# Kernel optimization log

Measured on AMD Instinct MI355X. Metric: run time of the kernel, lower is better.

## Reference

```python
import jax, jax.numpy as jnp
import numpy as np

D_DIM = 100000  # vocabulary size
W_DIM = 128     # embedding width
BATCH = 4096    # number of (center, context) index pairs


def setup_inputs() -> dict:
    key = jax.random.key(0)
    k1, k2, kw1, kb1, kw2, kb2 = jax.random.split(key, 6)
    idx1 = jax.random.randint(k1, (BATCH,), 0, D_DIM, dtype=jnp.int64 if jax.config.jax_enable_x64 else jnp.int32)
    idx2 = jax.random.randint(k2, (BATCH,), 0, D_DIM, dtype=jnp.int64 if jax.config.jax_enable_x64 else jnp.int32)
    # torch.nn.Linear(D, W): weight [W, D], bias [W], uniform(-1/sqrt(D), 1/sqrt(D))
    bound = 1.0 / np.sqrt(D_DIM)
    W1 = jax.random.uniform(kw1, (W_DIM, D_DIM), jnp.float32, -bound, bound)
    b1 = jax.random.uniform(kb1, (W_DIM,), jnp.float32, -bound, bound)
    W2 = jax.random.uniform(kw2, (W_DIM, D_DIM), jnp.float32, -bound, bound)
    b2 = jax.random.uniform(kb2, (W_DIM,), jnp.float32, -bound, bound)
    return {"idx1": idx1, "idx2": idx2, "W1": W1, "b1": b1, "W2": W2, "b2": b2}


def reference(idx1, idx2, W1, b1, W2, b2):
    # Linear(one_hot(idx)) == weight[:, idx] + bias  -> direct row (column) gather.
    p1 = W1[:, idx1].T + b1              # [B, W_dim]
    p2 = W2[:, idx2].T + b2              # [B, W_dim]
    s = jax.nn.sigmoid(jnp.sum(p1 * p2, axis=-1))  # [B]
    # original: cat([1 - sigmoid, sigmoid]) -> [B, 2]
    return jnp.stack([1.0 - s, s], axis=-1)
```

## Files before the change

### kernel.cpp

```cpp
#include <hip/hip_runtime.h>
#include <math.h>

#define D_DIM 100000
#define W_DIM 128
#define BATCH 4096

__global__ __launch_bounds__(256) void sgns_kernel(
    const int* __restrict__ idx1,
    const int* __restrict__ idx2,
    const float* __restrict__ W1,
    const float* __restrict__ b1,
    const float* __restrict__ W2,
    const float* __restrict__ b2,
    float* __restrict__ out)
{
    const int gtid = blockIdx.x * blockDim.x + threadIdx.x;
    const int wave = gtid >> 6;
    const int lane = gtid & 63;
    if (wave >= BATCH) return;

    const int i1 = idx1[wave];
    const int i2 = idx2[wave];

    const int w0 = lane;
    const int w1 = lane + 64;

    const float a0 = W1[w0 * D_DIM + i1];
    const float a1 = W1[w1 * D_DIM + i1];
    const float c0 = W2[w0 * D_DIM + i2];
    const float c1 = W2[w1 * D_DIM + i2];

    const float p0 = a0 + b1[w0];
    const float p1 = a1 + b1[w1];
    const float q0 = c0 + b2[w0];
    const float q1 = c1 + b2[w1];

    float v = p0 * q0 + p1 * q1;

    #pragma unroll
    for (int off = 32; off > 0; off >>= 1)
        v += __shfl_down(v, off, 64);

    if (lane == 0) {
        const float s = 1.0f / (1.0f + expf(-v));
        out[wave * 2 + 0] = 1.0f - s;
        out[wave * 2 + 1] = s;
    }
}

extern "C" void kernel_launch(void* const* d_in, const int* in_sizes, int n_in,
                              void* d_out, int out_size, void* d_ws, size_t ws_size,
                              hipStream_t stream)
{
    const int*   idx1 = (const int*)  d_in[0];
    const int*   idx2 = (const int*)  d_in[1];
    const float* W1   = (const float*)d_in[2];
    const float* b1   = (const float*)d_in[3];
    const float* W2   = (const float*)d_in[4];
    const float* b2   = (const float*)d_in[5];
    float* out = (float*)d_out;

    const int threads = 256;
    const int blocks  = (BATCH * 64) / threads;
    sgns_kernel<<<blocks, threads, 0, stream>>>(idx1, idx2, W1, b1, W2, b2, out);
}
```

Before: 125.3 us.

## Stream weight rows through LDS and gather indices, then reduce in second kernel

Replaces the scattered column gather with a two-kernel scheme. The first kernel streams contiguous chunks of each weight row into shared memory with coalesced float4 loads, then scatters the matching gathered values plus bias into a transposed workspace. The second kernel computes the dot products and the sigmoid from the workspace. This turns a random-access gather, where each element costs its own cache line, into a full sequential read of both weight matrices (about 102 MB). It adds a workspace round trip and a second launch, and the bandwidth cost no longer depends on batch size.

```diff
diff --git a/kernel.cpp b/kernel.cpp
--- a/kernel.cpp
+++ b/kernel.cpp
@@ -4,47 +4,70 @@
 #define D_DIM 100000
 #define W_DIM 128
 #define BATCH 4096
+#define CH    12288
+#define NCH   9
 
-__global__ __launch_bounds__(256) void sgns_kernel(
-    const int* __restrict__ idx1,
-    const int* __restrict__ idx2,
-    const float* __restrict__ W1,
-    const float* __restrict__ b1,
-    const float* __restrict__ W2,
-    const float* __restrict__ b2,
+__global__ __launch_bounds__(256) void gather_rows(
+    const int* __restrict__ idx1, const int* __restrict__ idx2,
+    const float* __restrict__ W1, const float* __restrict__ b1,
+    const float* __restrict__ W2, const float* __restrict__ b2,
+    float* __restrict__ G1T, float* __restrict__ G2T)
+{
+    __shared__ float lds[CH];
+
+    const int bid = blockIdx.x;
+    const int m   = bid / (W_DIM * NCH);
+    const int rem = bid % (W_DIM * NCH);
+    const int w   = rem / NCH;
+    const int c   = rem % NCH;
+
+    const float* __restrict__ W   = m ? W2   : W1;
+    const int*   __restrict__ idx = m ? idx2 : idx1;
+    const float  bias             = m ? b2[w] : b1[w];
+    float* __restrict__ GT        = m ? G2T  : G1T;
+
+    const int base  = c * CH;
+    const int limit = min(CH, D_DIM - base);
+    const float* src = W + (size_t)w * D_DIM + base;
+
+    const int n4 = limit >> 2;
+    const float4* __restrict__ src4 = (const float4*)src;
+    float4* lds4 = (float4*)lds;
+    for (int i = threadIdx.x; i < n4; i += 256)
+        lds4[i] = src4[i];
+    __syncthreads();
+
+    for (int b = threadIdx.x; b < BATCH; b += 256) {
+        const int rel = idx[b] - base;
+        if ((unsigned)rel < (unsigned)limit)
+            GT[w * BATCH + b] = lds[rel] + bias;
+    }
+}
+
+__global__ __launch_bounds__(256) void dot_sig(
+    const float* __restrict__ G1T, const float* __restrict__ G2T,
     float* __restrict__ out)
 {
-    const int gtid = blockIdx.x * blockDim.x + threadIdx.x;
-    const int wave = gtid >> 6;
-    const int lane = gtid & 63;
-    if (wave >= BATCH) return;
+    __shared__ float red[8][32];
+    const int bl = threadIdx.x & 31;
+    const int sl = threadIdx.x >> 5;
+    const int b  = blockIdx.x * 32 + bl;
 
-    const int i1 = idx1[wave];
-    const int i2 = idx2[wave];
+    float acc = 0.0f;
+    #pragma unroll
+    for (int k = 0; k < 16; ++k) {
+        const int w = sl * 16 + k;
+        acc += G1T[w * BATCH + b] * G2T[w * BATCH + b];
+    }
+    red[sl][bl] = acc;
+    __syncthreads();
 
-    const int w0 = lane;
-    const int w1 = lane + 64;
-
-    const float a0 = W1[w0 * D_DIM + i1];
-    const float a1 = W1[w1 * D_DIM + i1];
-    const float c0 = W2[w0 * D_DIM + i2];
-    const float c1 = W2[w1 * D_DIM + i2];
-
-    const float p0 = a0 + b1[w0];
-    const float p1 = a1 + b1[w1];
-    const float q0 = c0 + b2[w0];
-    const float q1 = c1 + b2[w1];
-
-    float v = p0 * q0 + p1 * q1;
-
-    #pragma unroll
-    for (int off = 32; off > 0; off >>= 1)
-        v += __shfl_down(v, off, 64);
-
-    if (lane == 0) {
-        const float s = 1.0f / (1.0f + expf(-v));
-        out[wave * 2 + 0] = 1.0f - s;
-        out[wave * 2 + 1] = s;
+    if (sl == 0) {
+        float v = 0.0f;
+        #pragma unroll
+        for (int s = 0; s < 8; ++s) v += red[s][bl];
+        const float sgm = 1.0f / (1.0f + expf(-v));
+        ((float2*)out)[b] = make_float2(1.0f - sgm, sgm);
     }
 }
 
@@ -60,7 +83,9 @@
     const float* b2   = (const float*)d_in[5];
     float* out = (float*)d_out;
 
-    const int threads = 256;
-    const int blocks  = (BATCH * 64) / threads;
-    sgns_kernel<<<blocks, threads, 0, stream>>>(idx1, idx2, W1, b1, W2, b2, out);
+    float* G1T = (float*)d_ws;
+    float* G2T = G1T + (size_t)W_DIM * BATCH;
+
+    gather_rows<<<2 * W_DIM * NCH, 256, 0, stream>>>(idx1, idx2, W1, b1, W2, b2, G1T, G2T);
+    dot_sig<<<BATCH / 32, 256, 0, stream>>>(G1T, G2T, out);
 }
```

Measured after the change: 151.9 us. +21.3%, slower.

## Bucket-sort indices to cluster column gathers, then split gather and dot into kernels

Applied to the files above, without the earlier changes.

Adds a single-block counting sort per index array that buckets indices by value (16 consecutive columns per bucket), so the gather kernel visits nearby columns of the weight matrices together and shares the 64-byte cache lines they touch. The gather kernel writes the biased embedding rows into a workspace buffer, and a separate kernel computes the dot product and sigmoid. The block order is swizzled to spread work. This costs two extra launches, a serial sort on only two blocks, and a round trip of 4 MB through the workspace buffer.

```diff
diff --git a/kernel.cpp b/kernel.cpp
--- a/kernel.cpp
+++ b/kernel.cpp
@@ -4,47 +4,103 @@
 #define D_DIM 100000
 #define W_DIM 128
 #define BATCH 4096
+#define NBUCK 6250
+#define BPAD  7168
 
-__global__ __launch_bounds__(256) void sgns_kernel(
-    const int* __restrict__ idx1,
-    const int* __restrict__ idx2,
-    const float* __restrict__ W1,
-    const float* __restrict__ b1,
-    const float* __restrict__ W2,
-    const float* __restrict__ b2,
-    float* __restrict__ out)
+__global__ __launch_bounds__(1024) void bucket_sort(
+    const int* __restrict__ idx1, const int* __restrict__ idx2,
+    unsigned int* __restrict__ packed)
 {
-    const int gtid = blockIdx.x * blockDim.x + threadIdx.x;
-    const int wave = gtid >> 6;
-    const int lane = gtid & 63;
-    if (wave >= BATCH) return;
+    __shared__ int cnt[BPAD];
+    __shared__ int ranks[BATCH];
+    __shared__ int psum[1024];
 
-    const int i1 = idx1[wave];
-    const int i2 = idx2[wave];
+    const int m = blockIdx.x;
+    const int* __restrict__ idx = m ? idx2 : idx1;
+    const int t = threadIdx.x;
 
-    const int w0 = lane;
-    const int w1 = lane + 64;
+    for (int i = t; i < BPAD; i += 1024) cnt[i] = 0;
+    __syncthreads();
 
-    const float a0 = W1[w0 * D_DIM + i1];
-    const float a1 = W1[w1 * D_DIM + i1];
-    const float c0 = W2[w0 * D_DIM + i2];
-    const float c1 = W2[w1 * D_DIM + i2];
+    for (int i = t; i < BATCH; i += 1024)
+        ranks[i] = atomicAdd(&cnt[idx[i] >> 4], 1);
+    __syncthreads();
 
-    const float p0 = a0 + b1[w0];
-    const float p1 = a1 + b1[w1];
-    const float q0 = c0 + b2[w0];
-    const float q1 = c1 + b2[w1];
+    const int base = t * 7;
+    int s = 0;
+    #pragma unroll
+    for (int j = 0; j < 7; ++j) s += cnt[base + j];
+    psum[t] = s;
+    __syncthreads();
 
-    float v = p0 * q0 + p1 * q1;
+    for (int off = 1; off < 1024; off <<= 1) {
+        int v = (t >= off) ? psum[t - off] : 0;
+        __syncthreads();
+        psum[t] += v;
+        __syncthreads();
+    }
+
+    int run = (t == 0) ? 0 : psum[t - 1];
+    #pragma unroll
+    for (int j = 0; j < 7; ++j) {
+        int c = cnt[base + j];
+        cnt[base + j] = run;
+        run += c;
+    }
+    __syncthreads();
+
+    for (int i = t; i < BATCH; i += 1024) {
+        const int v = idx[i];
+        const int pos = cnt[v >> 4] + ranks[i];
+        packed[m * BATCH + pos] = ((unsigned)v << 12) | (unsigned)i;
+    }
+}
+
+__global__ __launch_bounds__(256) void gather(
+    const unsigned int* __restrict__ packed,
+    const float* __restrict__ W1, const float* __restrict__ b1,
+    const float* __restrict__ W2, const float* __restrict__ b2,
+    float* __restrict__ P)
+{
+    const int bid   = blockIdx.x;
+    const int m     = bid >> 10;
+    const int local = bid & 1023;
+    const int nb = ((local & 7) << 7) | (local >> 3);
+    const int p  = (nb << 2) + (threadIdx.x >> 6);
+    const int l  = threadIdx.x & 63;
+
+    const unsigned int pk = packed[(m << 12) + p];
+    const int b = pk & 4095;
+    const int i = (int)(pk >> 12);
+
+    const float* __restrict__ W  = m ? W2 : W1;
+    const float* __restrict__ bb = m ? b2 : b1;
+
+    const float v0 = W[(size_t)l * D_DIM + i] + bb[l];
+    const float v1 = W[(size_t)(l + 64) * D_DIM + i] + bb[l + 64];
+
+    float* dst = P + (((size_t)(m << 12) + b) << 7);
+    dst[l]      = v0;
+    dst[l + 64] = v1;
+}
+
+__global__ __launch_bounds__(256) void dot_sig(
+    const float* __restrict__ P, float* __restrict__ out)
+{
+    const int b = (blockIdx.x << 2) + (threadIdx.x >> 6);
+    const int l = threadIdx.x & 63;
+
+    const float2 x = ((const float2*)(P + ((size_t)b << 7)))[l];
+    const float2 y = ((const float2*)(P + ((size_t)(BATCH + b) << 7)))[l];
+    float v = x.x * y.x + x.y * y.y;
 
     #pragma unroll
     for (int off = 32; off > 0; off >>= 1)
         v += __shfl_down(v, off, 64);
 
-    if (lane == 0) {
+    if (l == 0) {
         const float s = 1.0f / (1.0f + expf(-v));
-        out[wave * 2 + 0] = 1.0f - s;
-        out[wave * 2 + 1] = s;
+        ((float2*)out)[b] = make_float2(1.0f - s, s);
     }
 }
 
@@ -60,7 +116,10 @@
     const float* b2   = (const float*)d_in[5];
     float* out = (float*)d_out;
 
-    const int threads = 256;
-    const int blocks  = (BATCH * 64) / threads;
-    sgns_kernel<<<blocks, threads, 0, stream>>>(idx1, idx2, W1, b1, W2, b2, out);
+    unsigned int* packed = (unsigned int*)d_ws;
+    float* P = (float*)((char*)d_ws + 32768);
+
+    bucket_sort<<<2, 1024, 0, stream>>>(idx1, idx2, packed);
+    gather<<<2048, 256, 0, stream>>>(packed, W1, b1, W2, b2, P);
+    dot_sig<<<BATCH / 4, 256, 0, stream>>>(P, out);
 }
```

New measurement: 133.5 us. 1.07x slower.
